# Kernel tuning notes

Measured on AMD Instinct MI355X. Metric: run time of the kernel, lower is better.

The kernel has to match this reference:

```python
import jax, jax.numpy as jnp
import numpy as np


def setup_inputs() -> dict:
    key = jax.random.key(0)
    B, S, H, D = 2, 2048, 16, 64
    qkv = jax.random.normal(key, (B, S, 3, H, D), dtype=jnp.float32)
    return {"qkv_BxSx3xHxD": qkv}


def reference(qkv_BxSx3xHxD):
    # Two-step TTT with linear inner loop (eval mode: dropout_p = 0).
    q = qkv_BxSx3xHxD[:, :, 0]  # [B,S,H,D]
    k = qkv_BxSx3xHxD[:, :, 1]
    v = qkv_BxSx3xHxD[:, :, 2]
    # First causal linear-attention score matrix.
    a1 = jnp.tril(jnp.einsum('bthd,bshd->bhts', q, k))      # [B,H,S,S]
    # Intermediate output against K.
    o2 = jnp.einsum('bhts,bshd->bhtd', a1, k)                # [B,H,S,D]
    # Second causal score matrix from o2 vs K.
    a2 = jnp.tril(jnp.einsum('bhtd,bshd->bhts', o2, k))      # [B,H,S,S]
    a = 2.0 * a1 - a2                                        # fused correction
    return jnp.einsum('bhts,bshd->bthd', a, v)               # [B,S,H,D]
```

## Files before the change

kernel.cpp:

```cpp
#include <hip/hip_runtime.h>
#include <hip/hip_bf16.h>


typedef __bf16 bf16x8 __attribute__((ext_vector_type(8)));
typedef __bf16 bf16x2 __attribute__((ext_vector_type(2)));
typedef float  f32x4  __attribute__((ext_vector_type(4)));

#define MFMA16(a, b, c) __builtin_amdgcn_mfma_f32_16x16x32_bf16((a), (b), (c), 0, 0, 0)

static constexpr int S  = 2048;
static constexpr int H  = 16;
static constexpr int D  = 64;
static constexpr int RS = 3 * H * D;
static constexpr int BN = 64;
static constexpr int LR = 72;

__global__ __launch_bounds__(256, 3)
void ttt_kernel(const float* __restrict__ qkv, float* __restrict__ out)
{
    __shared__ __bf16 ldsK[2][BN * LR];
    __shared__ __bf16 ldsW[2][D  * LR];

    const int tid  = threadIdx.x;
    const int wv   = tid >> 6;
    const int lane = tid & 63;
    const int q    = lane >> 4;
    const int l16  = lane & 15;

    const int i  = (int)blockIdx.x;
    const int p  = 31 - (i >> 5);
    const int bh = i & 31;
    const int b  = bh >> 4;
    const int h  = bh & 15;
    const int t0 = 64 * p;
    const int nP = p + 1;

    const float* baseQ = qkv + (size_t)b * S * RS + h * D;
    const float* baseK = baseQ + H * D;
    const float* baseV = baseQ + 2 * H * D;

    const int r2  = (tid >> 3) * 2;
    const int cb  = (tid & 7) * 8;
    const int cbK = cb ^ (((r2 >> 3) & 1) << 5);

    f32x4 pk[4], pv[4];
    auto loadT = [&](f32x4* dst, const float* base, int s0) {
        const float* pg = base + (size_t)(s0 + r2) * RS + cb;
        dst[0] = *(const f32x4*)(pg);
        dst[1] = *(const f32x4*)(pg + 4);
        dst[2] = *(const f32x4*)(pg + RS);
        dst[3] = *(const f32x4*)(pg + RS + 4);
    };

    auto commit = [&](__bf16* K_, __bf16* W_, const f32x4* src) {
        bf16x8 w0, w1;
#pragma unroll
        for (int j = 0; j < 4; ++j) {
            w0[j] = (__bf16)pk[0][j]; w0[4 + j] = (__bf16)pk[1][j];
            w1[j] = (__bf16)pk[2][j]; w1[4 + j] = (__bf16)pk[3][j];
        }
        *(bf16x8*)(K_ + r2 * LR + cbK)       = w0;
        *(bf16x8*)(K_ + (r2 + 1) * LR + cbK) = w1;
#pragma unroll
        for (int j = 0; j < 8; ++j) {
            const int d = cb + j;
            bf16x2 w;
            w[0] = (__bf16)((j < 4) ? src[0][j & 3] : src[1][j & 3]);
            w[1] = (__bf16)((j < 4) ? src[2][j & 3] : src[3][j & 3]);
            *(bf16x2*)(W_ + d * LR + (r2 ^ (d & 56))) = w;
        }
    };

    loadT(pk, baseK, 0);

    bf16x8 Xf[2];
    const int row0 = wv * 16;
    {
        const float* pq = baseQ + (size_t)(t0 + row0 + l16) * RS + q * 8;
#pragma unroll
        for (int kt = 0; kt < 2; ++kt) {
            f32x4 f0 = *(const f32x4*)(pq + kt * 32);
            f32x4 f1 = *(const f32x4*)(pq + kt * 32 + 4);
#pragma unroll
            for (int j = 0; j < 4; ++j) {
                Xf[kt][j]     = (__bf16)f0[j];
                Xf[kt][4 + j] = (__bf16)f1[j];
            }
        }
    }

    const int rp   = (l16 >> 2) * 8 + (l16 & 3);
    const int kcol = (q * 8) | (((l16 >> 2) & 1) << 5);

    const f32x4 zero4 = {0.f, 0.f, 0.f, 0.f};
    f32x4 Y[4];
#pragma unroll
    for (int nd = 0; nd < 4; ++nd) Y[nd] = zero4;

    const int tg = t0 + wv * 16 + l16;

    commit(ldsK[0], ldsW[0], pk);
    __syncthreads();

    const int NT = 2 * nP;

    for (int u = 0; u < NT; ++u) {
        const int c  = u & 1;
        const int sb = (u >= nP) ? (u - nP) : u;

        if (u + 1 < NT) {
            const int np_ = (u + 1 >= nP) ? 1 : 0;
            const int nsb = (u + 1) - (np_ ? nP : 0);
            loadT(pk, baseK, nsb * BN);
            if (np_) loadT(pv, baseV, nsb * BN);
        }

        __bf16* K_ = ldsK[c];
        __bf16* W_ = ldsW[c];

        f32x4 Pt[4];
#pragma unroll
        for (int mi = 0; mi < 4; ++mi) Pt[mi] = zero4;
        __builtin_amdgcn_s_setprio(1);
#pragma unroll
        for (int kt = 0; kt < 2; ++kt) {
#pragma unroll
            for (int mi = 0; mi < 4; ++mi) {
                bf16x8 kf = *(bf16x8*)(K_
                    + ((mi >> 1) * 32 + (mi & 1) * 4 + rp) * LR
                    + ((kt * 32) ^ kcol));
                Pt[mi] = MFMA16(kf, Xf[kt], Pt[mi]);
            }
        }
        __builtin_amdgcn_s_setprio(0);

        bf16x8 wfr[2][4];
#pragma unroll
        for (int kt = 0; kt < 2; ++kt)
#pragma unroll
            for (int nd = 0; nd < 4; ++nd) {
                const int d = l16 + nd * 16;
                wfr[kt][nd] = *(bf16x8*)(W_ + d * LR + ((kt * 32 + q * 8) ^ (d & 56)));
            }

        bf16x8 af[2];
        {
            const bool diag = (sb == nP - 1);
#pragma unroll
            for (int kt = 0; kt < 2; ++kt) {
                bf16x8 a;
                if (diag) {
#pragma unroll
                    for (int b2 = 0; b2 < 2; ++b2)
#pragma unroll
                        for (int r = 0; r < 4; ++r) {
                            const int sg = sb * BN + kt * 32 + q * 8 + b2 * 4 + r;
                            a[b2 * 4 + r] = (sg <= tg) ? (__bf16)Pt[2 * kt + b2][r]
                                                       : (__bf16)0.0f;
                        }
                } else {
#pragma unroll
                    for (int b2 = 0; b2 < 2; ++b2)
#pragma unroll
                        for (int r = 0; r < 4; ++r)
                            a[b2 * 4 + r] = (__bf16)Pt[2 * kt + b2][r];
                }
                af[kt] = a;
            }
        }

        __builtin_amdgcn_s_setprio(1);
#pragma unroll
        for (int kt = 0; kt < 2; ++kt)
#pragma unroll
            for (int nd = 0; nd < 4; ++nd)
                Y[nd] = MFMA16(af[kt], wfr[kt][nd], Y[nd]);
        __builtin_amdgcn_s_setprio(0);

        if (u == nP - 1) {
            __bf16* sc = ldsW[1 - c] + row0 * LR;
#pragma unroll
            for (int nd = 0; nd < 4; ++nd)
#pragma unroll
                for (int r = 0; r < 4; ++r)
                    sc[(q * 4 + r) * LR + l16 + nd * 16] = (__bf16)Y[nd][r];
#pragma unroll
            for (int kt = 0; kt < 2; ++kt) {
                bf16x8 of = *(bf16x8*)(sc + l16 * LR + kt * 32 + q * 8);
#pragma unroll
                for (int j = 0; j < 8; ++j)
                    Xf[kt][j] = (__bf16)(2.0f * (float)Xf[kt][j] - (float)of[j]);
            }
#pragma unroll
            for (int nd = 0; nd < 4; ++nd) Y[nd] = zero4;
            __syncthreads();
        } else if (u == NT - 1) {
#pragma unroll
            for (int nd = 0; nd < 4; ++nd)
#pragma unroll
                for (int r = 0; r < 4; ++r) {
                    const int t = t0 + wv * 16 + q * 4 + r;
                    const int d = l16 + nd * 16;
                    out[(((size_t)b * S + t) * H + h) * D + d] = Y[nd][r];
                }
        }

        if (u + 1 < NT) {
            commit(ldsK[1 - c], ldsW[1 - c], (u + 1 >= nP) ? pv : pk);
            __syncthreads();
        }
    }
}

extern "C" void kernel_launch(void* const* d_in, const int* in_sizes, int n_in,
                              void* d_out, int out_size, void* d_ws, size_t ws_size,
                              hipStream_t stream)
{
    const float* qkv = (const float*)d_in[0];
    float* out = (float*)d_out;
    ttt_kernel<<<dim3(1024), 256, 0, stream>>>(qkv, out);
}
```

Before: 136.9 us.

## Halve waves per block, give each wave two 16-row query groups

Cuts the block to 128 threads (2 waves), with each wave handling 32 query rows as two 16-row groups. Each K fragment read from LDS now feeds two MFMAs, and each W fragment is reused across both groups, which roughly halves LDS fragment reads per MFMA. Each thread also loads and commits four rows instead of two. The cost is more registers per thread (doubled accumulators and prefetch buffers) and fewer waves per block for latency hiding.

```diff
diff --git a/kernel.cpp b/kernel.cpp
--- a/kernel.cpp
+++ b/kernel.cpp
@@ -3,7 +3,7 @@
 
 
 typedef __bf16 bf16x8 __attribute__((ext_vector_type(8)));
-typedef __bf16 bf16x2 __attribute__((ext_vector_type(2)));
+typedef __bf16 bf16x4 __attribute__((ext_vector_type(4)));
 typedef float  f32x4  __attribute__((ext_vector_type(4)));
 
 #define MFMA16(a, b, c) __builtin_amdgcn_mfma_f32_16x16x32_bf16((a), (b), (c), 0, 0, 0)
@@ -15,7 +15,7 @@
 static constexpr int BN = 64;
 static constexpr int LR = 72;
 
-__global__ __launch_bounds__(256, 3)
+__global__ __launch_bounds__(128, 2)
 void ttt_kernel(const float* __restrict__ qkv, float* __restrict__ out)
 {
     __shared__ __bf16 ldsK[2][BN * LR];
@@ -39,52 +39,56 @@
     const float* baseK = baseQ + H * D;
     const float* baseV = baseQ + 2 * H * D;
 
-    const int r2  = (tid >> 3) * 2;
+    const int r4  = (tid >> 3) * 4;
     const int cb  = (tid & 7) * 8;
-    const int cbK = cb ^ (((r2 >> 3) & 1) << 5);
-
-    f32x4 pk[4], pv[4];
+    const int cbK = cb ^ (((r4 >> 3) & 1) << 5);
+
+    f32x4 pk[8], pv[8];
     auto loadT = [&](f32x4* dst, const float* base, int s0) {
-        const float* pg = base + (size_t)(s0 + r2) * RS + cb;
-        dst[0] = *(const f32x4*)(pg);
-        dst[1] = *(const f32x4*)(pg + 4);
-        dst[2] = *(const f32x4*)(pg + RS);
-        dst[3] = *(const f32x4*)(pg + RS + 4);
+        const float* pg = base + (size_t)(s0 + r4) * RS + cb;
+#pragma unroll
+        for (int r = 0; r < 4; ++r) {
+            dst[2 * r]     = *(const f32x4*)(pg + r * RS);
+            dst[2 * r + 1] = *(const f32x4*)(pg + r * RS + 4);
+        }
     };
 
-    auto commit = [&](__bf16* K_, __bf16* W_, const f32x4* src) {
-        bf16x8 w0, w1;
-#pragma unroll
-        for (int j = 0; j < 4; ++j) {
-            w0[j] = (__bf16)pk[0][j]; w0[4 + j] = (__bf16)pk[1][j];
-            w1[j] = (__bf16)pk[2][j]; w1[4 + j] = (__bf16)pk[3][j];
-        }
-        *(bf16x8*)(K_ + r2 * LR + cbK)       = w0;
-        *(bf16x8*)(K_ + (r2 + 1) * LR + cbK) = w1;
+    auto commit = [&](__bf16* K_, __bf16* W_, const f32x4* ksrc, const f32x4* wsrc) {
+#pragma unroll
+        for (int r = 0; r < 4; ++r) {
+            bf16x8 w;
+#pragma unroll
+            for (int j = 0; j < 4; ++j) {
+                w[j]     = (__bf16)ksrc[2 * r][j];
+                w[4 + j] = (__bf16)ksrc[2 * r + 1][j];
+            }
+            *(bf16x8*)(K_ + (r4 + r) * LR + cbK) = w;
+        }
 #pragma unroll
         for (int j = 0; j < 8; ++j) {
             const int d = cb + j;
-            bf16x2 w;
-            w[0] = (__bf16)((j < 4) ? src[0][j & 3] : src[1][j & 3]);
-            w[1] = (__bf16)((j < 4) ? src[2][j & 3] : src[3][j & 3]);
-            *(bf16x2*)(W_ + d * LR + (r2 ^ (d & 56))) = w;
+            bf16x4 w;
+#pragma unroll
+            for (int r = 0; r < 4; ++r)
+                w[r] = (__bf16)wsrc[2 * r + (j >> 2)][j & 3];
+            *(bf16x4*)(W_ + d * LR + (r4 ^ (d & 56))) = w;
         }
     };
 
     loadT(pk, baseK, 0);
 
-    bf16x8 Xf[2];
-    const int row0 = wv * 16;
-    {
-        const float* pq = baseQ + (size_t)(t0 + row0 + l16) * RS + q * 8;
+    bf16x8 Xf[2][2];
+#pragma unroll
+    for (int g = 0; g < 2; ++g) {
+        const float* pq = baseQ + (size_t)(t0 + wv * 32 + g * 16 + l16) * RS + q * 8;
 #pragma unroll
         for (int kt = 0; kt < 2; ++kt) {
             f32x4 f0 = *(const f32x4*)(pq + kt * 32);
             f32x4 f1 = *(const f32x4*)(pq + kt * 32 + 4);
 #pragma unroll
             for (int j = 0; j < 4; ++j) {
-                Xf[kt][j]     = (__bf16)f0[j];
-                Xf[kt][4 + j] = (__bf16)f1[j];
+                Xf[g][kt][j]     = (__bf16)f0[j];
+                Xf[g][kt][4 + j] = (__bf16)f1[j];
             }
         }
     }
@@ -93,13 +97,15 @@
     const int kcol = (q * 8) | (((l16 >> 2) & 1) << 5);
 
     const f32x4 zero4 = {0.f, 0.f, 0.f, 0.f};
-    f32x4 Y[4];
-#pragma unroll
-    for (int nd = 0; nd < 4; ++nd) Y[nd] = zero4;
-
-    const int tg = t0 + wv * 16 + l16;
-
-    commit(ldsK[0], ldsW[0], pk);
+    f32x4 Y[2][4];
+#pragma unroll
+    for (int g = 0; g < 2; ++g)
+#pragma unroll
+        for (int nd = 0; nd < 4; ++nd) Y[g][nd] = zero4;
+
+    const int tg0 = t0 + wv * 32 + l16;
+
+    commit(ldsK[0], ldsW[0], pk, pk);
     __syncthreads();
 
     const int NT = 2 * nP;
@@ -118,9 +124,11 @@
         __bf16* K_ = ldsK[c];
         __bf16* W_ = ldsW[c];
 
-        f32x4 Pt[4];
-#pragma unroll
-        for (int mi = 0; mi < 4; ++mi) Pt[mi] = zero4;
+        f32x4 Pt[2][4];
+#pragma unroll
+        for (int g = 0; g < 2; ++g)
+#pragma unroll
+            for (int mi = 0; mi < 4; ++mi) Pt[g][mi] = zero4;
         __builtin_amdgcn_s_setprio(1);
 #pragma unroll
         for (int kt = 0; kt < 2; ++kt) {
@@ -129,7 +137,8 @@
                 bf16x8 kf = *(bf16x8*)(K_
                     + ((mi >> 1) * 32 + (mi & 1) * 4 + rp) * LR
                     + ((kt * 32) ^ kcol));
-                Pt[mi] = MFMA16(kf, Xf[kt], Pt[mi]);
+                Pt[0][mi] = MFMA16(kf, Xf[0][kt], Pt[0][mi]);
+                Pt[1][mi] = MFMA16(kf, Xf[1][kt], Pt[1][mi]);
             }
         }
         __builtin_amdgcn_s_setprio(0);
@@ -143,29 +152,33 @@
                 wfr[kt][nd] = *(bf16x8*)(W_ + d * LR + ((kt * 32 + q * 8) ^ (d & 56)));
             }
 
-        bf16x8 af[2];
+        bf16x8 af[2][2];
         {
             const bool diag = (sb == nP - 1);
 #pragma unroll
-            for (int kt = 0; kt < 2; ++kt) {
-                bf16x8 a;
-                if (diag) {
-#pragma unroll
-                    for (int b2 = 0; b2 < 2; ++b2)
-#pragma unroll
-                        for (int r = 0; r < 4; ++r) {
-                            const int sg = sb * BN + kt * 32 + q * 8 + b2 * 4 + r;
-                            a[b2 * 4 + r] = (sg <= tg) ? (__bf16)Pt[2 * kt + b2][r]
-                                                       : (__bf16)0.0f;
-                        }
-                } else {
-#pragma unroll
-                    for (int b2 = 0; b2 < 2; ++b2)
-#pragma unroll
-                        for (int r = 0; r < 4; ++r)
-                            a[b2 * 4 + r] = (__bf16)Pt[2 * kt + b2][r];
+            for (int g = 0; g < 2; ++g) {
+                const int tg = tg0 + g * 16;
+#pragma unroll
+                for (int kt = 0; kt < 2; ++kt) {
+                    bf16x8 a;
+                    if (diag) {
+#pragma unroll
+                        for (int b2 = 0; b2 < 2; ++b2)
+#pragma unroll
+                            for (int r = 0; r < 4; ++r) {
+                                const int sg = sb * BN + kt * 32 + q * 8 + b2 * 4 + r;
+                                a[b2 * 4 + r] = (sg <= tg) ? (__bf16)Pt[g][2 * kt + b2][r]
+                                                           : (__bf16)0.0f;
+                            }
+                    } else {
+#pragma unroll
+                        for (int b2 = 0; b2 < 2; ++b2)
+#pragma unroll
+                            for (int r = 0; r < 4; ++r)
+                                a[b2 * 4 + r] = (__bf16)Pt[g][2 * kt + b2][r];
+                    }
+                    af[g][kt] = a;
                 }
-                af[kt] = a;
             }
         }
 
@@ -173,40 +186,50 @@
 #pragma unroll
         for (int kt = 0; kt < 2; ++kt)
 #pragma unroll
-            for (int nd = 0; nd < 4; ++nd)
-                Y[nd] = MFMA16(af[kt], wfr[kt][nd], Y[nd]);
+            for (int nd = 0; nd < 4; ++nd) {
+                Y[0][nd] = MFMA16(af[0][kt], wfr[kt][nd], Y[0][nd]);
+                Y[1][nd] = MFMA16(af[1][kt], wfr[kt][nd], Y[1][nd]);
+            }
         __builtin_amdgcn_s_setprio(0);
 
         if (u == nP - 1) {
-            __bf16* sc = ldsW[1 - c] + row0 * LR;
-#pragma unroll
-            for (int nd = 0; nd < 4; ++nd)
-#pragma unroll
-                for (int r = 0; r < 4; ++r)
-                    sc[(q * 4 + r) * LR + l16 + nd * 16] = (__bf16)Y[nd][r];
-#pragma unroll
-            for (int kt = 0; kt < 2; ++kt) {
-                bf16x8 of = *(bf16x8*)(sc + l16 * LR + kt * 32 + q * 8);
-#pragma unroll
-                for (int j = 0; j < 8; ++j)
-                    Xf[kt][j] = (__bf16)(2.0f * (float)Xf[kt][j] - (float)of[j]);
-            }
-#pragma unroll
-            for (int nd = 0; nd < 4; ++nd) Y[nd] = zero4;
+            __bf16* sc = ldsW[1 - c] + (wv * 32) * LR;
+#pragma unroll
+            for (int g = 0; g < 2; ++g)
+#pragma unroll
+                for (int nd = 0; nd < 4; ++nd)
+#pragma unroll
+                    for (int r = 0; r < 4; ++r)
+                        sc[(g * 16 + q * 4 + r) * LR + l16 + nd * 16] = (__bf16)Y[g][nd][r];
+#pragma unroll
+            for (int g = 0; g < 2; ++g)
+#pragma unroll
+                for (int kt = 0; kt < 2; ++kt) {
+                    bf16x8 of = *(bf16x8*)(sc + (g * 16 + l16) * LR + kt * 32 + q * 8);
+#pragma unroll
+                    for (int j = 0; j < 8; ++j)
+                        Xf[g][kt][j] = (__bf16)(2.0f * (float)Xf[g][kt][j] - (float)of[j]);
+                }
+#pragma unroll
+            for (int g = 0; g < 2; ++g)
+#pragma unroll
+                for (int nd = 0; nd < 4; ++nd) Y[g][nd] = zero4;
             __syncthreads();
         } else if (u == NT - 1) {
 #pragma unroll
-            for (int nd = 0; nd < 4; ++nd)
-#pragma unroll
-                for (int r = 0; r < 4; ++r) {
-                    const int t = t0 + wv * 16 + q * 4 + r;
-                    const int d = l16 + nd * 16;
-                    out[(((size_t)b * S + t) * H + h) * D + d] = Y[nd][r];
-                }
+            for (int g = 0; g < 2; ++g)
+#pragma unroll
+                for (int nd = 0; nd < 4; ++nd)
+#pragma unroll
+                    for (int r = 0; r < 4; ++r) {
+                        const int t = t0 + wv * 32 + g * 16 + q * 4 + r;
+                        const int d = l16 + nd * 16;
+                        out[(((size_t)b * S + t) * H + h) * D + d] = Y[g][nd][r];
+                    }
         }
 
         if (u + 1 < NT) {
-            commit(ldsK[1 - c], ldsW[1 - c], (u + 1 >= nP) ? pv : pk);
+            commit(ldsK[1 - c], ldsW[1 - c], pk, (u + 1 >= nP) ? pv : pk);
             __syncthreads();
         }
     }
@@ -218,5 +241,5 @@
 {
     const float* qkv = (const float*)d_in[0];
     float* out = (float*)d_out;
-    ttt_kernel<<<dim3(1024), 256, 0, stream>>>(qkv, out);
+    ttt_kernel<<<dim3(1024), 128, 0, stream>>>(qkv, out);
 }
```

Result: slower. 151.9 us (+11.0%).
